# Optimization experiments

Measured on AMD Instinct MI355X. Metric: run time of the kernel, lower is better.

## Reference

```python
import jax, jax.numpy as jnp
import numpy as np

K = 3
ALPHA = 8.3

def _patches(x, oh, ow):
    # x: [B, C, H, W] -> [B, C, K, K, oh, ow] (stride=1, dilation=1)
    rows = []
    for k in range(K):
        cols = [x[:, :, k:k + oh, l:l + ow] for l in range(K)]
        rows.append(jnp.stack(cols, axis=2))  # [B, C, K, oh, ow]
    return jnp.stack(rows, axis=2)  # [B, C, K, K, oh, ow]

def setup_inputs() -> dict:
    key = jax.random.key(0)
    k1, k2, k3, k4 = jax.random.split(key, 4)
    B, C, H, W = 4, 64, 256, 256
    OC = 64
    img = jax.random.normal(k1, (B, C, H, W), dtype=jnp.float32)
    depth = jax.random.uniform(k2, (B, 1, H, W), dtype=jnp.float32)
    weight = jax.random.uniform(k3, (OC, C, K, K), dtype=jnp.float32, minval=-0.1, maxval=0.1)
    bias = jax.random.uniform(k4, (1, OC), dtype=jnp.float32, minval=-0.1, maxval=0.1)
    return {"img": img, "depth": depth, "weight": weight, "bias": bias}

def reference(img, depth, weight, bias):
    B, C, H, W = img.shape
    oh, ow = H - K + 1, W - K + 1
    c0 = K // 2
    img_p = _patches(img, oh, ow)                 # [B, C, K, K, oh, ow]
    dep_p = _patches(depth, oh, ow)[:, 0]         # [B, K, K, oh, ow]
    center = depth[:, 0, c0:c0 + oh, c0:c0 + ow]  # [B, oh, ow]
    dw = jnp.exp(-ALPHA * jnp.abs(dep_p - center[:, None, None]))  # [B, K, K, oh, ow]
    out = jnp.einsum('bcklpq,bklpq,ockl->bopq', img_p, dw, weight)
    out = out + bias[0][None, :, None, None]
    return out
```

## Files before the change

kernel.cpp:

```cpp
#include <hip/hip_runtime.h>
#include <hip/hip_bf16.h>

typedef __bf16 bf16_t;
typedef __bf16 bf16x8 __attribute__((ext_vector_type(8)));
typedef float f32x4 __attribute__((ext_vector_type(4)));

#define ALPHA 8.3f

__global__ void repack_w(const float* __restrict__ w, bf16_t* __restrict__ w2) {
    int idx = blockIdx.x * 256 + threadIdx.x;
    if (idx >= 9 * 2 * 4 * 64 * 8) return;
    int j     = idx & 7;
    int lane  = (idx >> 3) & 63;
    int m     = (idx >> 9) & 3;
    int chunk = (idx >> 11) & 1;
    int tap   = idx >> 12;
    int oc = m * 16 + (lane & 15);
    int c  = chunk * 32 + (lane >> 4) * 8 + j;
    int kt = tap / 3, lt = tap % 3;
    w2[idx] = (bf16_t)w[((oc * 64 + c) * 3 + kt) * 3 + lt];
}

__global__ __launch_bounds__(256) void depthconv_mfma(
    const float* __restrict__ img, const float* __restrict__ depth,
    const bf16_t* __restrict__ w2, const float* __restrict__ bias,
    float* __restrict__ out)
{
    const int wv   = threadIdx.x >> 6;
    const int lane = threadIdx.x & 63;
    const int n    = lane & 15;
    const int quad = lane >> 4;

    int t   = blockIdx.x * 4 + wv;
    int tq  = t & 3;
    int p   = (t >> 2) % 254;
    int b   = (t >> 2) / 254;
    int q0  = (tq == 3) ? 190 : tq * 64;

    const float* dep  = depth + (size_t)b * 65536;
    const float* imgb = img + (size_t)b * 64 * 65536;

    float dc[4];
#pragma unroll
    for (int i = 0; i < 4; ++i)
        dc[i] = dep[(p + 1) * 256 + (q0 + i * 16 + n + 1)];

    f32x4 acc[4][4];
#pragma unroll
    for (int m = 0; m < 4; ++m)
#pragma unroll
        for (int i = 0; i < 4; ++i)
            acc[m][i] = (f32x4){0.f, 0.f, 0.f, 0.f};

    for (int kt = 0; kt < 3; ++kt) {
        for (int lt = 0; lt < 3; ++lt) {
            const int tap = kt * 3 + lt;
            float dwv[4];
#pragma unroll
            for (int i = 0; i < 4; ++i) {
                float d = dep[(p + kt) * 256 + (q0 + i * 16 + n + lt)];
                dwv[i] = __expf(-ALPHA * fabsf(d - dc[i]));
            }
#pragma unroll
            for (int chunk = 0; chunk < 2; ++chunk) {
                bf16x8 a[4];
                const bf16x8* w2p =
                    (const bf16x8*)w2 + ((size_t)(tap * 2 + chunk) * 4) * 64 + lane;
#pragma unroll
                for (int m = 0; m < 4; ++m) a[m] = w2p[m * 64];

                const float* ip = imgb
                    + (size_t)(chunk * 32 + quad * 8) * 65536
                    + (size_t)(p + kt) * 256 + (q0 + n + lt);
#pragma unroll
                for (int i = 0; i < 4; ++i) {
                    bf16x8 bf;
#pragma unroll
                    for (int j = 0; j < 8; ++j)
                        bf[j] = (bf16_t)(ip[(size_t)j * 65536 + i * 16] * dwv[i]);
#pragma unroll
                    for (int m = 0; m < 4; ++m)
                        acc[m][i] = __builtin_amdgcn_mfma_f32_16x16x32_bf16(
                            a[m], bf, acc[m][i], 0, 0, 0);
                }
            }
        }
    }

#pragma unroll
    for (int m = 0; m < 4; ++m) {
#pragma unroll
        for (int r = 0; r < 4; ++r) {
            int oc = m * 16 + quad * 4 + r;
            float bz = bias[oc];
#pragma unroll
            for (int i = 0; i < 4; ++i) {
                int q = q0 + i * 16 + n;
                out[((size_t)(b * 64 + oc) * 254 + p) * 254 + q] = acc[m][i][r] + bz;
            }
        }
    }
}

extern "C" void kernel_launch(void* const* d_in, const int* in_sizes, int n_in,
                              void* d_out, int out_size, void* d_ws, size_t ws_size,
                              hipStream_t stream) {
    const float* img   = (const float*)d_in[0];
    const float* depth = (const float*)d_in[1];
    const float* w     = (const float*)d_in[2];
    const float* bias  = (const float*)d_in[3];
    bf16_t* w2 = (bf16_t*)d_ws;

    repack_w<<<144, 256, 0, stream>>>(w, w2);
    depthconv_mfma<<<1016, 256, 0, stream>>>(img, depth, w2, bias, (float*)d_out);
}
```

Baseline: 179.2 us.

## Stage bf16 image rows in LDS and apply depth weights after MFMA

Measured after the change: 176.9 us. Within noise of the previous version (-1.3%).

```diff
diff --git a/kernel.cpp b/kernel.cpp
--- a/kernel.cpp
+++ b/kernel.cpp
@@ -2,10 +2,14 @@
 #include <hip/hip_bf16.h>
 
 typedef __bf16 bf16_t;
+typedef __bf16 bf16x4 __attribute__((ext_vector_type(4)));
 typedef __bf16 bf16x8 __attribute__((ext_vector_type(8)));
 typedef float f32x4 __attribute__((ext_vector_type(4)));
 
 #define ALPHA 8.3f
+#define CPAD 72
+#define NCOL 136
+
 
 __global__ void repack_w(const float* __restrict__ w, bf16_t* __restrict__ w2) {
     int idx = blockIdx.x * 256 + threadIdx.x;
@@ -21,29 +25,53 @@
     w2[idx] = (bf16_t)w[((oc * 64 + c) * 3 + kt) * 3 + lt];
 }
 
-__global__ __launch_bounds__(256) void depthconv_mfma(
+__global__ __launch_bounds__(128) void depthconv_mfma(
     const float* __restrict__ img, const float* __restrict__ depth,
     const bf16_t* __restrict__ w2, const float* __restrict__ bias,
     float* __restrict__ out)
 {
-    const int wv   = threadIdx.x >> 6;
-    const int lane = threadIdx.x & 63;
+    __shared__ bf16_t lds[3 * NCOL * CPAD];
+
+    const int tid = threadIdx.x;
+    const int p = blockIdx.x >> 3;
+    const int r = blockIdx.x & 7;
+    const int b = r >> 1;
+    const int h = r & 1;
+    const int s0 = h ? 120 : 0;
+
+    const float* imgb = img + (size_t)b * 64 * 65536;
+    const float* dep  = depth + (size_t)b * 65536;
+
+    for (int u = tid; u < 3 * 34 * 16; u += 128) {
+        int cg   = u & 15;
+        int colg = (u >> 4) % 34;
+        int kt   = (u >> 4) / 34;
+        int c0  = cg * 4;
+        int cl0 = colg * 4;
+        const float* src = imgb + (size_t)c0 * 65536 + (p + kt) * 256 + s0 + cl0;
+        float4 v0 = *(const float4*)src;
+        float4 v1 = *(const float4*)(src + 65536);
+        float4 v2 = *(const float4*)(src + 2 * 65536);
+        float4 v3 = *(const float4*)(src + 3 * 65536);
+        bf16_t* dst = lds + (size_t)(kt * NCOL + cl0) * CPAD + c0;
+        *(bf16x4*)(dst)            = (bf16x4){(bf16_t)v0.x, (bf16_t)v1.x, (bf16_t)v2.x, (bf16_t)v3.x};
+        *(bf16x4*)(dst + CPAD)     = (bf16x4){(bf16_t)v0.y, (bf16_t)v1.y, (bf16_t)v2.y, (bf16_t)v3.y};
+        *(bf16x4*)(dst + 2 * CPAD) = (bf16x4){(bf16_t)v0.z, (bf16_t)v1.z, (bf16_t)v2.z, (bf16_t)v3.z};
+        *(bf16x4*)(dst + 3 * CPAD) = (bf16x4){(bf16_t)v0.w, (bf16_t)v1.w, (bf16_t)v2.w, (bf16_t)v3.w};
+    }
+    __syncthreads();
+
+    const int wv   = tid >> 6;
+    const int lane = tid & 63;
     const int n    = lane & 15;
     const int quad = lane >> 4;
-
-    int t   = blockIdx.x * 4 + wv;
-    int tq  = t & 3;
-    int p   = (t >> 2) % 254;
-    int b   = (t >> 2) / 254;
-    int q0  = (tq == 3) ? 190 : tq * 64;
-
-    const float* dep  = depth + (size_t)b * 65536;
-    const float* imgb = img + (size_t)b * 64 * 65536;
+    const int q0w  = h * 126 + wv * 64;
+    const int clb0 = q0w - s0;
 
     float dc[4];
 #pragma unroll
     for (int i = 0; i < 4; ++i)
-        dc[i] = dep[(p + 1) * 256 + (q0 + i * 16 + n + 1)];
+        dc[i] = dep[(p + 1) * 256 + q0w + 16 * i + n + 1];
 
     f32x4 acc[4][4];
 #pragma unroll
@@ -51,52 +79,61 @@
 #pragma unroll
         for (int i = 0; i < 4; ++i)
             acc[m][i] = (f32x4){0.f, 0.f, 0.f, 0.f};
+    const f32x4 Z = (f32x4){0.f, 0.f, 0.f, 0.f};
 
     for (int kt = 0; kt < 3; ++kt) {
+        float dwv[3][4];
+#pragma unroll
+        for (int lt = 0; lt < 3; ++lt)
+#pragma unroll
+            for (int i = 0; i < 4; ++i) {
+                float d = dep[(p + kt) * 256 + q0w + 16 * i + n + lt];
+                dwv[lt][i] = __expf(-ALPHA * fabsf(d - dc[i]));
+            }
+#pragma unroll
         for (int lt = 0; lt < 3; ++lt) {
             const int tap = kt * 3 + lt;
-            float dwv[4];
-#pragma unroll
-            for (int i = 0; i < 4; ++i) {
-                float d = dep[(p + kt) * 256 + (q0 + i * 16 + n + lt)];
-                dwv[i] = __expf(-ALPHA * fabsf(d - dc[i]));
-            }
+            f32x4 P[4][4];
 #pragma unroll
             for (int chunk = 0; chunk < 2; ++chunk) {
                 bf16x8 a[4];
-                const bf16x8* w2p =
-                    (const bf16x8*)w2 + ((size_t)(tap * 2 + chunk) * 4) * 64 + lane;
+                const bf16x8* w2p = (const bf16x8*)w2 + ((size_t)(tap * 2 + chunk) * 4) * 64 + lane;
 #pragma unroll
                 for (int m = 0; m < 4; ++m) a[m] = w2p[m * 64];
-
-                const float* ip = imgb
-                    + (size_t)(chunk * 32 + quad * 8) * 65536
-                    + (size_t)(p + kt) * 256 + (q0 + n + lt);
 #pragma unroll
                 for (int i = 0; i < 4; ++i) {
-                    bf16x8 bf;
+                    const bf16x8 bf = *(const bf16x8*)(
+                        lds + (size_t)(kt * NCOL + clb0 + 16 * i + n + lt) * CPAD
+                            + chunk * 32 + quad * 8);
+                    if (chunk == 0) {
 #pragma unroll
-                    for (int j = 0; j < 8; ++j)
-                        bf[j] = (bf16_t)(ip[(size_t)j * 65536 + i * 16] * dwv[i]);
+                        for (int m = 0; m < 4; ++m)
+                            P[m][i] = __builtin_amdgcn_mfma_f32_16x16x32_bf16(a[m], bf, Z, 0, 0, 0);
+                    } else {
 #pragma unroll
-                    for (int m = 0; m < 4; ++m)
-                        acc[m][i] = __builtin_amdgcn_mfma_f32_16x16x32_bf16(
-                            a[m], bf, acc[m][i], 0, 0, 0);
+                        for (int m = 0; m < 4; ++m)
+                            P[m][i] = __builtin_amdgcn_mfma_f32_16x16x32_bf16(a[m], bf, P[m][i], 0, 0, 0);
+                    }
                 }
             }
+#pragma unroll
+            for (int m = 0; m < 4; ++m)
+#pragma unroll
+                for (int i = 0; i < 4; ++i)
+                    acc[m][i] += dwv[lt][i] * P[m][i];
         }
     }
 
 #pragma unroll
     for (int m = 0; m < 4; ++m) {
 #pragma unroll
-        for (int r = 0; r < 4; ++r) {
-            int oc = m * 16 + quad * 4 + r;
+        for (int r2 = 0; r2 < 4; ++r2) {
+            int oc = m * 16 + quad * 4 + r2;
             float bz = bias[oc];
 #pragma unroll
             for (int i = 0; i < 4; ++i) {
-                int q = q0 + i * 16 + n;
-                out[((size_t)(b * 64 + oc) * 254 + p) * 254 + q] = acc[m][i][r] + bz;
+                int q = q0w + 16 * i + n;
+                out[((size_t)(b * 64 + oc) * 254 + p) * 254 + q] = acc[m][i][r2] + bz;
             }
         }
     }
@@ -112,5 +149,5 @@
     bf16_t* w2 = (bf16_t*)d_ws;
 
     repack_w<<<144, 256, 0, stream>>>(w, w2);
-    depthconv_mfma<<<1016, 256, 0, stream>>>(img, depth, w2, bias, (float*)d_out);
+    depthconv_mfma<<<2032, 128, 0, stream>>>(img, depth, w2, bias, (float*)d_out);
 }
```
